# Kernel optimization log

Hardware: AMD Instinct MI355X
Metric: run time of the kernel (lower is better)

The kernel has to match this reference:

```python
import jax, jax.numpy as jnp
import numpy as np

B, N, D = 2, 2048, 1024
H = 16
DP = D // H          # projection dim per head = 64
SCALE = DP ** 0.5

def setup_inputs() -> dict:
    key = jax.random.key(0)
    ks = jax.random.split(key, 5)
    s_in = 1.0 / np.sqrt(D)
    s_merge = 1.0 / np.sqrt(H * DP)
    x = jax.random.normal(ks[0], (B, N, D), dtype=jnp.float32)
    W_qkv = jax.random.normal(ks[1], (D, 3 * H * DP), dtype=jnp.float32) * s_in
    b_qkv = jnp.zeros((3 * H * DP,), dtype=jnp.float32)
    W_out = jax.random.normal(ks[2], (H * DP, D), dtype=jnp.float32) * s_merge
    b_out = jnp.zeros((D,), dtype=jnp.float32)
    return {"x": x, "W_qkv": W_qkv, "b_qkv": b_qkv, "W_out": W_out, "b_out": b_out}

def reference(x, W_qkv, b_qkv, W_out, b_out):
    # packed QKV projection: (B,N,3*H*DP)
    qkv = jnp.einsum("bnd,de->bne", x, W_qkv) + b_qkv
    # reshape to (B,N,H,3*DP) -> (B,H,N,3*DP), split along last axis
    qkv = qkv.reshape(B, N, H, 3 * DP).transpose(0, 2, 1, 3)
    q, k, v = jnp.split(qkv, 3, axis=-1)                 # each (B,H,N,DP)
    scores = jnp.einsum("bhqd,bhkd->bhqk", q, k) / SCALE  # (B,H,N,N)
    attn = jax.nn.softmax(scores, axis=-1)
    out = jnp.einsum("bhqk,bhkd->bhqd", attn, v)          # (B,H,N,DP)
    out = out.transpose(0, 2, 1, 3).reshape(B, N, H * DP)
    return jnp.einsum("bne,ed->bnd", out, W_out) + b_out
```

## Files before the change

### kernel.cpp

```cpp
#include <hip/hip_runtime.h>
#include <hip/hip_bf16.h>

#define BB 2
#define NN 2048
#define DD 1024
#define HH 16
#define DP 64

typedef __attribute__((ext_vector_type(8))) short short8;
typedef __attribute__((ext_vector_type(4))) short short4v;
typedef __attribute__((ext_vector_type(4))) float float4v;

static __device__ __forceinline__ short f2bf(float f) {
  union { float f; unsigned u; } v; v.f = f;
  unsigned r = v.u + 0x7fffu + ((v.u >> 16) & 1u);
  return (short)(r >> 16);
}

static __device__ __forceinline__ void gload16(const void* g, void* l) {
  __builtin_amdgcn_global_load_lds(
      (const __attribute__((address_space(1))) void*)g,
      (__attribute__((address_space(3))) void*)l, 16, 0, 0);
}

__global__ __launch_bounds__(256) void prep(
    const float* __restrict__ x, short* __restrict__ xb,
    const float* __restrict__ Wqkv, short* __restrict__ wqkt,
    const float* __restrict__ Wout, short* __restrict__ wott) {
  __shared__ short tile[32][33];
  const int b = blockIdx.x, t = threadIdx.x;
  if (b < 4096) {
    int i = (b * 256 + t) * 4;
    float4v f = *(const float4v*)(x + i);
    short4v s;
#pragma unroll
    for (int j = 0; j < 4; ++j) s[j] = f2bf(f[j]);
    *(short4v*)(xb + i) = s;
    return;
  }
  const float* in;  short* out;  int R, C, bx, by;
  if (b < 7168) { int idx = b - 4096; bx = idx % 96; by = idx / 96;
                  in = Wqkv; out = wqkt; R = 1024; C = 3072; }
  else          { int idx = b - 7168; bx = idx % 32; by = idx / 32;
                  in = Wout; out = wott; R = 1024; C = 1024; }
  int c0 = bx * 32, r0 = by * 32;
  int tx = t & 31, ty = t >> 5;
#pragma unroll
  for (int i = 0; i < 32; i += 8)
    tile[ty + i][tx] = f2bf(in[(size_t)(r0 + ty + i) * C + c0 + tx]);
  __syncthreads();
#pragma unroll
  for (int i = 0; i < 32; i += 8)
    out[(size_t)(c0 + ty + i) * R + r0 + tx] = tile[tx][ty + i];
}

__global__ __launch_bounds__(256, 6) void gemm_qkv_mfma(
    const short* __restrict__ A, const short* __restrict__ Bt,
    const float* __restrict__ bias,
    short* __restrict__ Qb, short* __restrict__ Kb, short* __restrict__ Vtb) {
  __shared__ short As[2][64 * 32];
  __shared__ short Bs[2][128 * 32];
  const int K = DD;
  const int t = threadIdx.x;
  const int w = t >> 6, lane = t & 63;
  const int l16 = lane & 15, quad = lane >> 4;
  const int wm = w >> 1, wn = w & 1;
  const int bm0 = blockIdx.y * 64;
  const int bn0 = blockIdx.x * 128;
  const int rA = lane >> 2, cA = lane & 3;
  const short* aRow  = A  + (size_t)(bm0 + w * 16 + rA) * K + cA * 8;
  const short* bRow0 = Bt + (size_t)(bn0 + w * 16 + rA) * K + cA * 8;
  const short* bRow1 = Bt + (size_t)(bn0 + 64 + w * 16 + rA) * K + cA * 8;
  char* AsB = (char*)&As[0][0] + w * 1024;
  char* BsB = (char*)&Bs[0][0] + w * 1024;
  float4v acc[2][4] = {};

  gload16(aRow, AsB);
  gload16(bRow0, BsB);
  gload16(bRow1, BsB + 4096);
  __syncthreads();

  int cur = 0;
  for (int k0 = 0; k0 < K; k0 += 32) {
    if (k0 + 32 < K) {
      const int nxt = cur ^ 1;
      gload16(aRow + k0 + 32, AsB + nxt * 4096);
      gload16(bRow0 + k0 + 32, BsB + nxt * 8192);
      gload16(bRow1 + k0 + 32, BsB + nxt * 8192 + 4096);
    }
    short8 af[2], bf[4];
#pragma unroll
    for (int mb = 0; mb < 2; ++mb)
      af[mb] = *(const short8*)&As[cur][((wm * 32 + mb * 16 + l16) * 4 + quad) * 8];
#pragma unroll
    for (int nb = 0; nb < 4; ++nb)
      bf[nb] = *(const short8*)&Bs[cur][((wn * 64 + nb * 16 + l16) * 4 + quad) * 8];
#pragma unroll
    for (int mb = 0; mb < 2; ++mb)
#pragma unroll
      for (int nb = 0; nb < 4; ++nb)
        acc[mb][nb] = __builtin_amdgcn_mfma_f32_16x16x32_bf16(af[mb], bf[nb],
                                                              acc[mb][nb], 0, 0, 0);
    __syncthreads();
    cur ^= 1;
  }

#pragma unroll
  for (int mb = 0; mb < 2; ++mb)
#pragma unroll
    for (int nb = 0; nb < 4; ++nb)
#pragma unroll
      for (int r = 0; r < 4; ++r) {
        int m = bm0 + wm * 32 + mb * 16 + quad * 4 + r;
        int e = bn0 + wn * 64 + nb * 16 + l16;
        float v = acc[mb][nb][r] + bias[e];
        int b_ = m >> 11;
        int n = m & 2047;
        int h = e / 192;
        int rr = e - h * 192;
        int which = rr >> 6;
        int d = rr & 63;
        if (which == 0)      Qb[((b_ * HH + h) * NN + n) * DP + d] = f2bf(v * 0.125f);
        else if (which == 1) Kb[((b_ * HH + h) * NN + n) * DP + d] = f2bf(v);
        else                 Vtb[((b_ * HH + h) * DP + d) * NN + n] = f2bf(v);
      }
}

__global__ __launch_bounds__(256, 4) void gemm_out_mfma(
    const short* __restrict__ A, const short* __restrict__ Bt,
    const float* __restrict__ bias, float* __restrict__ C) {
  __shared__ short As[2][64 * 32];
  __shared__ short Bs[2][64 * 32];
  const int K = DD;
  const int t = threadIdx.x;
  const int w = t >> 6, lane = t & 63;
  const int l16 = lane & 15, quad = lane >> 4;
  const int wm = w >> 1, wn = w & 1;
  const int bm0 = blockIdx.y * 64;
  const int bn0 = blockIdx.x * 64;
  const int rA = lane >> 2, cA = lane & 3;
  const short* aRow = A  + (size_t)(bm0 + w * 16 + rA) * K + cA * 8;
  const short* bRow = Bt + (size_t)(bn0 + w * 16 + rA) * K + cA * 8;
  char* AsB = (char*)&As[0][0] + w * 1024;
  char* BsB = (char*)&Bs[0][0] + w * 1024;
  float4v acc[2][2] = {};

  gload16(aRow, AsB);
  gload16(bRow, BsB);
  __syncthreads();

  int cur = 0;
  for (int k0 = 0; k0 < K; k0 += 32) {
    if (k0 + 32 < K) {
      const int nxt = cur ^ 1;
      gload16(aRow + k0 + 32, AsB + nxt * 4096);
      gload16(bRow + k0 + 32, BsB + nxt * 4096);
    }
    short8 af[2], bf[2];
#pragma unroll
    for (int mb = 0; mb < 2; ++mb)
      af[mb] = *(const short8*)&As[cur][((wm * 32 + mb * 16 + l16) * 4 + quad) * 8];
#pragma unroll
    for (int nb = 0; nb < 2; ++nb)
      bf[nb] = *(const short8*)&Bs[cur][((wn * 32 + nb * 16 + l16) * 4 + quad) * 8];
#pragma unroll
    for (int mb = 0; mb < 2; ++mb)
#pragma unroll
      for (int nb = 0; nb < 2; ++nb)
        acc[mb][nb] = __builtin_amdgcn_mfma_f32_16x16x32_bf16(af[mb], bf[nb],
                                                              acc[mb][nb], 0, 0, 0);
    __syncthreads();
    cur ^= 1;
  }

#pragma unroll
  for (int mb = 0; mb < 2; ++mb)
#pragma unroll
    for (int nb = 0; nb < 2; ++nb)
#pragma unroll
      for (int r = 0; r < 4; ++r) {
        int m = bm0 + wm * 32 + mb * 16 + quad * 4 + r;
        int e = bn0 + wn * 32 + nb * 16 + l16;
        C[(size_t)m * DD + e] = acc[mb][nb][r] + bias[e];
      }
}

#define QT 64
#define KT 64
#define FIXMAX 16.0f

__global__ __launch_bounds__(256, 4) void attn_mfma(
    const short* __restrict__ Qb, const short* __restrict__ Kb,
    const short* __restrict__ Vtb, short* __restrict__ Ob) {
  __shared__ short Ks[2][4096];
  __shared__ short Vs[2][4096];
  __shared__ short Ps[4][16 * 64];

  const int t = threadIdx.x;
  const int w = t >> 6;
  const int lane = t & 63;
  const int l16 = lane & 15;
  const int quad = lane >> 4;
  const int bh = blockIdx.y;
  const int q0 = blockIdx.x * QT + w * 16;
  const size_t base  = (size_t)bh * NN * DP;
  const size_t baseT = (size_t)bh * DP * NN;

  short8 qa0, qa1;
  {
    const short* qp = Qb + base + (size_t)(q0 + l16) * DP + quad * 8;
    qa0 = *(const short8*)(qp);
    qa1 = *(const short8*)(qp + 32);
  }

  float4v o_acc[4] = {};
  float l_part[4] = {0.f, 0.f, 0.f, 0.f};

  short* myP = &Ps[w][0];
  const int swz = (l16 & 7) << 3;

  const int rKV = lane >> 2;
  const int qd = lane & 3;
  char* KsB = (char*)&Ks[0][0] + w * 1024;
  char* VsB = (char*)&Vs[0][0] + w * 1024;
  const short* kRow = Kb + base + (size_t)(w * 16 + rKV) * DP + qd * 8;
  const short* vRow = Vtb + baseT + (size_t)(w * 16 + rKV) * NN + qd * 8;

  gload16(kRow, KsB);
  gload16(kRow + 32, KsB + 4096);
  gload16(vRow, VsB);
  gload16(vRow + 32, VsB + 4096);
  __syncthreads();

  int cur = 0;
  for (int k0 = 0; k0 < NN; k0 += KT) {
    if (k0 + KT < NN) {
      const int nxt = cur ^ 1;
      gload16(kRow + (size_t)(k0 + KT) * DP, KsB + nxt * 8192);
      gload16(kRow + (size_t)(k0 + KT) * DP + 32, KsB + nxt * 8192 + 4096);
      gload16(vRow + k0 + KT, VsB + nxt * 8192);
      gload16(vRow + k0 + KT + 32, VsB + nxt * 8192 + 4096);
    }
    const short* Kc = &Ks[cur][0];
    const short* Vc = &Vs[cur][0];

    float4v s_acc[4] = {};
#pragma unroll
    for (int nb = 0; nb < 4; ++nb) {
      short8 b0 = *(const short8*)(Kc + nb * 512 + l16 * 32 + quad * 8);
      short8 b1 = *(const short8*)(Kc + 2048 + nb * 512 + l16 * 32 + quad * 8);
      s_acc[nb] = __builtin_amdgcn_mfma_f32_16x16x32_bf16(qa0, b0, s_acc[nb], 0, 0, 0);
      s_acc[nb] = __builtin_amdgcn_mfma_f32_16x16x32_bf16(qa1, b1, s_acc[nb], 0, 0, 0);
    }

#pragma unroll
    for (int nb = 0; nb < 4; ++nb)
#pragma unroll
      for (int r = 0; r < 4; ++r) {
        float p = __expf(s_acc[nb][r] - FIXMAX);
        l_part[r] += p;
        union { float f; unsigned u; } v; v.f = p;
        int row = quad * 4 + r;
        myP[row * 64 + ((nb * 16 + l16) ^ ((row & 7) << 3))] =
            (short)((v.u + 0x8000u) >> 16);
      }

    const short* pp = myP + l16 * 64;
    short8 pa0 = *(const short8*)(pp + ((quad * 8) ^ swz));
    short8 pa1 = *(const short8*)(pp + ((32 + quad * 8) ^ swz));

#pragma unroll
    for (int db = 0; db < 4; ++db) {
      short8 v0 = *(const short8*)(Vc + db * 512 + l16 * 32 + quad * 8);
      short8 v1 = *(const short8*)(Vc + 2048 + db * 512 + l16 * 32 + quad * 8);
      o_acc[db] = __builtin_amdgcn_mfma_f32_16x16x32_bf16(pa0, v0, o_acc[db], 0, 0, 0);
      o_acc[db] = __builtin_amdgcn_mfma_f32_16x16x32_bf16(pa1, v1, o_acc[db], 0, 0, 0);
    }

    __syncthreads();
    cur ^= 1;
  }

  const int b_ = bh >> 4, h = bh & 15;
  float inv_l[4];
#pragma unroll
  for (int r = 0; r < 4; ++r) {
    float s = l_part[r];
    s += __shfl_xor(s, 1);
    s += __shfl_xor(s, 2);
    s += __shfl_xor(s, 4);
    s += __shfl_xor(s, 8);
    inv_l[r] = 1.0f / s;
  }
#pragma unroll
  for (int db = 0; db < 4; ++db)
#pragma unroll
    for (int r = 0; r < 4; ++r) {
      int row = q0 + quad * 4 + r;
      Ob[(size_t)(b_ * NN + row) * (HH * DP) + h * DP + db * 16 + l16] =
          f2bf(o_acc[db][r] * inv_l[r]);
    }
}

extern "C" void kernel_launch(void* const* d_in, const int* in_sizes, int n_in,
                              void* d_out, int out_size, void* d_ws, size_t ws_size,
                              hipStream_t stream) {
  const float* x    = (const float*)d_in[0];
  const float* Wqkv = (const float*)d_in[1];
  const float* bqkv = (const float*)d_in[2];
  const float* Wout = (const float*)d_in[3];
  const float* bout = (const float*)d_in[4];
  float* out = (float*)d_out;

  const int nQKV = BB * HH * NN * DP;
  const int nX   = BB * NN * DD;
  short* qb   = (short*)d_ws;
  short* kb   = qb + nQKV;
  short* vtb  = kb + nQKV;
  short* ob   = vtb + nQKV;
  short* xb   = ob + nQKV;
  short* wqkt = xb + nX;
  short* wott = wqkt + 3 * HH * DP * DD;

  prep<<<4096 + 3072 + 1024, 256, 0, stream>>>(x, xb, Wqkv, wqkt, Wout, wott);

  gemm_qkv_mfma<<<dim3(3 * HH * DP / 128, BB * NN / 64), 256, 0, stream>>>(
      xb, wqkt, bqkv, qb, kb, vtb);
  attn_mfma<<<dim3(NN / QT, BB * HH), 256, 0, stream>>>(qb, kb, vtb, ob);
  gemm_out_mfma<<<dim3(DD / 64, BB * NN / 64), 256, 0, stream>>>(
      ob, wott, bout, out);
}
```

Baseline: 221.8 us.

## Rewrite attention with 32x32x16 MFMA, register-resident P, and direct global K/V loads

Restructures the attention kernel around 32x32x16 bf16 MFMAs computing S^T = K·Q^T, so the P tile stays in registers. A cross-half lane shuffle rearranges P into operand layout, removing the LDS round trip and per-tile __syncthreads. K and V fragments are now read straight from global memory each iteration instead of being double-buffered through LDS. Each wave now handles 32 queries (128 per block, half the grid), and launch bounds drop to 2 blocks per SM. The risk is higher global/L2 traffic from redundant K/V reads across waves and lower occupancy from more registers, with no explicit prefetch to hide load latency.

```diff
diff --git a/kernel.cpp b/kernel.cpp
--- a/kernel.cpp
+++ b/kernel.cpp
@@ -10,6 +10,7 @@
 typedef __attribute__((ext_vector_type(8))) short short8;
 typedef __attribute__((ext_vector_type(4))) short short4v;
 typedef __attribute__((ext_vector_type(4))) float float4v;
+typedef __attribute__((ext_vector_type(16))) float f32x16;
 
 static __device__ __forceinline__ short f2bf(float f) {
   union { float f; unsigned u; } v; v.f = f;
@@ -185,120 +186,106 @@
       }
 }
 
-#define QT 64
-#define KT 64
 #define FIXMAX 16.0f
 
-__global__ __launch_bounds__(256, 4) void attn_mfma(
+__global__ __launch_bounds__(256, 2) void attn_mfma(
     const short* __restrict__ Qb, const short* __restrict__ Kb,
     const short* __restrict__ Vtb, short* __restrict__ Ob) {
-  __shared__ short Ks[2][4096];
-  __shared__ short Vs[2][4096];
-  __shared__ short Ps[4][16 * 64];
-
   const int t = threadIdx.x;
   const int w = t >> 6;
   const int lane = t & 63;
-  const int l16 = lane & 15;
-  const int quad = lane >> 4;
+  const int l31 = lane & 31;
+  const int hi = lane >> 5;
   const int bh = blockIdx.y;
-  const int q0 = blockIdx.x * QT + w * 16;
+  const int q0 = blockIdx.x * 128 + w * 32;
   const size_t base  = (size_t)bh * NN * DP;
   const size_t baseT = (size_t)bh * DP * NN;
 
-  short8 qa0, qa1;
+  short8 qf[4];
   {
-    const short* qp = Qb + base + (size_t)(q0 + l16) * DP + quad * 8;
-    qa0 = *(const short8*)(qp);
-    qa1 = *(const short8*)(qp + 32);
-  }
-
-  float4v o_acc[4] = {};
-  float l_part[4] = {0.f, 0.f, 0.f, 0.f};
-
-  short* myP = &Ps[w][0];
-  const int swz = (l16 & 7) << 3;
-
-  const int rKV = lane >> 2;
-  const int qd = lane & 3;
-  char* KsB = (char*)&Ks[0][0] + w * 1024;
-  char* VsB = (char*)&Vs[0][0] + w * 1024;
-  const short* kRow = Kb + base + (size_t)(w * 16 + rKV) * DP + qd * 8;
-  const short* vRow = Vtb + baseT + (size_t)(w * 16 + rKV) * NN + qd * 8;
-
-  gload16(kRow, KsB);
-  gload16(kRow + 32, KsB + 4096);
-  gload16(vRow, VsB);
-  gload16(vRow + 32, VsB + 4096);
-  __syncthreads();
-
-  int cur = 0;
-  for (int k0 = 0; k0 < NN; k0 += KT) {
-    if (k0 + KT < NN) {
-      const int nxt = cur ^ 1;
-      gload16(kRow + (size_t)(k0 + KT) * DP, KsB + nxt * 8192);
-      gload16(kRow + (size_t)(k0 + KT) * DP + 32, KsB + nxt * 8192 + 4096);
-      gload16(vRow + k0 + KT, VsB + nxt * 8192);
-      gload16(vRow + k0 + KT + 32, VsB + nxt * 8192 + 4096);
-    }
-    const short* Kc = &Ks[cur][0];
-    const short* Vc = &Vs[cur][0];
-
-    float4v s_acc[4] = {};
-#pragma unroll
-    for (int nb = 0; nb < 4; ++nb) {
-      short8 b0 = *(const short8*)(Kc + nb * 512 + l16 * 32 + quad * 8);
-      short8 b1 = *(const short8*)(Kc + 2048 + nb * 512 + l16 * 32 + quad * 8);
-      s_acc[nb] = __builtin_amdgcn_mfma_f32_16x16x32_bf16(qa0, b0, s_acc[nb], 0, 0, 0);
-      s_acc[nb] = __builtin_amdgcn_mfma_f32_16x16x32_bf16(qa1, b1, s_acc[nb], 0, 0, 0);
-    }
-
-#pragma unroll
-    for (int nb = 0; nb < 4; ++nb)
-#pragma unroll
-      for (int r = 0; r < 4; ++r) {
-        float p = __expf(s_acc[nb][r] - FIXMAX);
-        l_part[r] += p;
-        union { float f; unsigned u; } v; v.f = p;
-        int row = quad * 4 + r;
-        myP[row * 64 + ((nb * 16 + l16) ^ ((row & 7) << 3))] =
-            (short)((v.u + 0x8000u) >> 16);
+    const short* qp = Qb + base + (size_t)(q0 + l31) * DP + hi * 8;
+#pragma unroll
+    for (int c = 0; c < 4; ++c) qf[c] = *(const short8*)(qp + c * 16);
+  }
+
+  f32x16 oacc[2] = {};
+  float l_loc = 0.f;
+
+  const short* kp = Kb  + base  + (size_t)l31 * DP + hi * 8;
+  const short* vp = Vtb + baseT + (size_t)l31 * NN + hi * 8;
+
+  for (int k0 = 0; k0 < NN; k0 += 64) {
+    short8 kf[2][4];
+#pragma unroll
+    for (int nb = 0; nb < 2; ++nb)
+#pragma unroll
+      for (int c = 0; c < 4; ++c)
+        kf[nb][c] = *(const short8*)(kp + (size_t)(k0 + nb * 32) * DP + c * 16);
+
+    f32x16 sacc[2] = {};
+#pragma unroll
+    for (int c = 0; c < 4; ++c) {
+      sacc[0] = __builtin_amdgcn_mfma_f32_32x32x16_bf16(kf[0][c], qf[c], sacc[0], 0, 0, 0);
+      sacc[1] = __builtin_amdgcn_mfma_f32_32x32x16_bf16(kf[1][c], qf[c], sacc[1], 0, 0, 0);
+    }
+
+    short8 vf[2][4];
+#pragma unroll
+    for (int db = 0; db < 2; ++db)
+#pragma unroll
+      for (int c = 0; c < 4; ++c)
+        vf[db][c] = *(const short8*)(vp + (size_t)(db * 32) * NN + k0 + c * 16);
+
+    short8 pb[4];
+#pragma unroll
+    for (int b = 0; b < 2; ++b) {
+      float pe[16];
+#pragma unroll
+      for (int r = 0; r < 16; ++r) {
+        pe[r] = __expf(sacc[b][r] - FIXMAX);
+        l_loc += pe[r];
       }
-
-    const short* pp = myP + l16 * 64;
-    short8 pa0 = *(const short8*)(pp + ((quad * 8) ^ swz));
-    short8 pa1 = *(const short8*)(pp + ((32 + quad * 8) ^ swz));
-
-#pragma unroll
-    for (int db = 0; db < 4; ++db) {
-      short8 v0 = *(const short8*)(Vc + db * 512 + l16 * 32 + quad * 8);
-      short8 v1 = *(const short8*)(Vc + 2048 + db * 512 + l16 * 32 + quad * 8);
-      o_acc[db] = __builtin_amdgcn_mfma_f32_16x16x32_bf16(pa0, v0, o_acc[db], 0, 0, 0);
-      o_acc[db] = __builtin_amdgcn_mfma_f32_16x16x32_bf16(pa1, v1, o_acc[db], 0, 0, 0);
-    }
-
-    __syncthreads();
-    cur ^= 1;
+      unsigned W[8];
+#pragma unroll
+      for (int j = 0; j < 8; ++j)
+        W[j] = (unsigned)(unsigned short)f2bf(pe[2 * j]) |
+               ((unsigned)(unsigned short)f2bf(pe[2 * j + 1]) << 16);
+      unsigned tw[8];
+#pragma unroll
+      for (int j = 0; j < 8; ++j) tw[j] = (unsigned)__shfl_xor((int)W[j], 32);
+      union { unsigned u[4]; short8 s; } f0, f1;
+      f0.u[0] = hi ? tw[2] : W[0];
+      f0.u[1] = hi ? tw[3] : W[1];
+      f0.u[2] = hi ? W[2] : tw[0];
+      f0.u[3] = hi ? W[3] : tw[1];
+      f1.u[0] = hi ? tw[6] : W[4];
+      f1.u[1] = hi ? tw[7] : W[5];
+      f1.u[2] = hi ? W[6] : tw[4];
+      f1.u[3] = hi ? W[7] : tw[5];
+      pb[2 * b]     = f0.s;
+      pb[2 * b + 1] = f1.s;
+    }
+
+#pragma unroll
+    for (int c = 0; c < 4; ++c) {
+      oacc[0] = __builtin_amdgcn_mfma_f32_32x32x16_bf16(vf[0][c], pb[c], oacc[0], 0, 0, 0);
+      oacc[1] = __builtin_amdgcn_mfma_f32_32x32x16_bf16(vf[1][c], pb[c], oacc[1], 0, 0, 0);
+    }
   }
 
   const int b_ = bh >> 4, h = bh & 15;
-  float inv_l[4];
-#pragma unroll
-  for (int r = 0; r < 4; ++r) {
-    float s = l_part[r];
-    s += __shfl_xor(s, 1);
-    s += __shfl_xor(s, 2);
-    s += __shfl_xor(s, 4);
-    s += __shfl_xor(s, 8);
-    inv_l[r] = 1.0f / s;
-  }
-#pragma unroll
-  for (int db = 0; db < 4; ++db)
-#pragma unroll
-    for (int r = 0; r < 4; ++r) {
-      int row = q0 + quad * 4 + r;
-      Ob[(size_t)(b_ * NN + row) * (HH * DP) + h * DP + db * 16 + l16] =
-          f2bf(o_acc[db][r] * inv_l[r]);
+  const float l_tot = l_loc + __shfl_xor(l_loc, 32);
+  const float inv = 1.0f / l_tot;
+  const int q = q0 + l31;
+  short* orow = Ob + (size_t)(b_ * NN + q) * (HH * DP) + h * DP;
+#pragma unroll
+  for (int db = 0; db < 2; ++db)
+#pragma unroll
+    for (int g = 0; g < 4; ++g) {
+      short4v s4;
+#pragma unroll
+      for (int e = 0; e < 4; ++e) s4[e] = f2bf(oacc[db][g * 4 + e] * inv);
+      *(short4v*)(orow + db * 32 + g * 8 + hi * 4) = s4;
     }
 }
 
@@ -326,7 +313,7 @@
 
   gemm_qkv_mfma<<<dim3(3 * HH * DP / 128, BB * NN / 64), 256, 0, stream>>>(
       xb, wqkt, bqkv, qb, kb, vtb);
-  attn_mfma<<<dim3(NN / QT, BB * HH), 256, 0, stream>>>(qb, kb, vtb, ob);
+  attn_mfma<<<dim3(NN / 128, BB * HH), 256, 0, stream>>>(qb, kb, vtb, ob);
   gemm_out_mfma<<<dim3(DD / 64, BB * NN / 64), 256, 0, stream>>>(
       ob, wott, bout, out);
 }
```

Measured after the change: 271.5 us. 1.22x slower.
